# Performance work log

Measured on AMD Instinct MI355X. Metric: run time of the kernel, lower is better.

## Reference

```python
import jax, jax.numpy as jnp
import numpy as np

B, L, KD, ED, H = 8, 4096, 512, 1024, 8  # batch, seq, key_dim, embed_dim, n_heads
LN_EPS = 1e-5


def setup_inputs() -> dict:
    key = jax.random.key(0)
    ks = jax.random.split(key, 6)
    keys = jax.random.normal(ks[0], (B, L, KD), dtype=jnp.float32)
    values = jax.random.normal(ks[1], (B, L, ED), dtype=jnp.float32)
    # learned params
    query = jax.random.normal(ks[2], (H, 1, KD // H), dtype=jnp.float32) * 0.02
    k_bias = jax.random.normal(ks[3], (KD,), dtype=jnp.float32) / np.sqrt(KD).astype(np.float32)
    v_bias = jnp.zeros((ED,), dtype=jnp.float32)
    softmax_weight = 1.0 + 0.01 * jax.random.normal(ks[4], (H, 1, L + 1), dtype=jnp.float32)
    softmax_bias = 0.01 * jax.random.normal(ks[5], (H, 1, L + 1), dtype=jnp.float32)
    gamma = jnp.ones((ED,), dtype=jnp.float32)
    beta = jnp.zeros((ED,), dtype=jnp.float32)
    return {"keys": keys, "values": values, "query": query, "k_bias": k_bias,
            "v_bias": v_bias, "softmax_weight": softmax_weight,
            "softmax_bias": softmax_bias, "gamma": gamma, "beta": beta}


def reference(keys, values, query, k_bias, v_bias, softmax_weight, softmax_bias, gamma, beta):
    b = keys.shape[0]
    # append learned bias token to keys and values  -> [B, L+1, *]
    keys = jnp.concatenate([keys, jnp.broadcast_to(k_bias, (b, 1, k_bias.shape[0]))], axis=1)
    values = jnp.concatenate([values, jnp.broadcast_to(v_bias, (b, 1, v_bias.shape[0]))], axis=1)
    lp = keys.shape[1]
    # torch multihead_reshape is a raw contiguous view [B,L,C] -> [B*H, L, C/H]
    K = keys.reshape(b * H, lp, keys.shape[2] // H)      # [B*H, L+1, KD/H]
    V = values.reshape(b * H, lp, values.shape[2] // H)  # [B*H, L+1, ED/H]
    Q = jnp.tile(query, (b, 1, 1))                       # [B*H, 1, KD/H]
    scores = jnp.einsum('bqd,bld->bql', Q, K)            # [B*H, 1, L+1]
    scores = scores * jnp.tile(softmax_weight, (b, 1, 1)) + jnp.tile(softmax_bias, (b, 1, 1))
    attn = jax.nn.softmax(scores, axis=-1)               # [B*H, 1, L+1]
    A = jnp.einsum('bql,bld->bqd', attn, V)              # [B*H, 1, ED/H]
    A = A.reshape(b, 1, -1)                              # multihead_unshape -> [B, 1, ED]
    # LayerNorm over embed dim (torch default eps=1e-5, biased var)
    mean = jnp.mean(A, axis=-1, keepdims=True)
    var = jnp.var(A, axis=-1, keepdims=True)
    return (A - mean) * jax.lax.rsqrt(var + LN_EPS) * gamma + beta
```

## Files before the change

### kernel.cpp

```cpp
#include <hip/hip_runtime.h>

#define BATCH 8
#define LSEQ  4096
#define LP    4097
#define KDIM  512
#define EDIM  1024
#define NH    8
#define DK    64
#define DV    128
#define NG    64
#define NCH   16
#define KLIM  (LSEQ * KDIM)
#define VLIM  (LSEQ * EDIM)
#define LN_EPS 1e-5f

typedef float floatx4 __attribute__((ext_vector_type(4)));

#define STAGE_LOAD(S, rr) do {                                              \
    const int rk0 = (rr) + gid;                                             \
    const int rk1 = (rr) + 4 + gid;                                         \
    const int f0 = fheadk + rk0 * DK;                                       \
    const int f1 = fheadk + rk1 * DK;                                       \
    const float* p0 = (f0 < KLIM) ? (kp + f0) : (k_bias + (f0 - KLIM));     \
    const float* p1 = (f1 < KLIM) ? (kp + f1) : (k_bias + (f1 - KLIM));     \
    kv0##S = *reinterpret_cast<const floatx4*>(p0 + l16 * 4);               \
    kv1##S = *reinterpret_cast<const floatx4*>(p1 + l16 * 4);               \
    wv0##S = wptr[rk0]; bv0##S = bptr[rk0];                                 \
    wv1##S = wptr[rk1]; bv1##S = bptr[rk1];                                 \
    _Pragma("unroll")                                                       \
    for (int j = 0; j < 4; ++j) {                                           \
        const int fv = fheadv + ((rr) + 2 * j + hi) * DV;                   \
        const float* pv = (fv < VLIM) ? (vp + fv) : (v_bias + (fv - VLIM)); \
        vv##S[j] = *reinterpret_cast<const floatx4*>(pv + d0);              \
    }                                                                       \
} while (0)

#define STAGE_COMPUTE(S) do {                                               \
    float s0 = q.x * kv0##S.x + q.y * kv0##S.y + q.z * kv0##S.z + q.w * kv0##S.w; \
    float s1 = q.x * kv1##S.x + q.y * kv1##S.y + q.z * kv1##S.z + q.w * kv1##S.w; \
    s0 += __shfl_xor(s0, 1); s1 += __shfl_xor(s1, 1);                       \
    s0 += __shfl_xor(s0, 2); s1 += __shfl_xor(s1, 2);                       \
    s0 += __shfl_xor(s0, 4); s1 += __shfl_xor(s1, 4);                       \
    s0 += __shfl_xor(s0, 8); s1 += __shfl_xor(s1, 8);                       \
    const float e0 = __expf(s0 * wv0##S + bv0##S);                          \
    const float e1 = __expf(s1 * wv1##S + bv1##S);                          \
    z += e0 + e1;                                                           \
    const float w0 = __shfl(e0, 16 * hi, 64);                               \
    const float w1 = __shfl(e0, 16 * (2 + hi), 64);                         \
    const float w2 = __shfl(e1, 16 * hi, 64);                               \
    const float w3 = __shfl(e1, 16 * (2 + hi), 64);                         \
    a0 += w0 * vv##S[0].x; a1 += w0 * vv##S[0].y;                           \
    a2 += w0 * vv##S[0].z; a3 += w0 * vv##S[0].w;                           \
    a0 += w1 * vv##S[1].x; a1 += w1 * vv##S[1].y;                           \
    a2 += w1 * vv##S[1].z; a3 += w1 * vv##S[1].w;                           \
    a0 += w2 * vv##S[2].x; a1 += w2 * vv##S[2].y;                           \
    a2 += w2 * vv##S[2].z; a3 += w2 * vv##S[2].w;                           \
    a0 += w3 * vv##S[3].x; a1 += w3 * vv##S[3].y;                           \
    a2 += w3 * vv##S[3].z; a3 += w3 * vv##S[3].w;                           \
} while (0)

#define SB __builtin_amdgcn_sched_barrier(0)

__global__ __launch_bounds__(256, 4) void lqa_fused_kernel(
    const float* __restrict__ keys, const float* __restrict__ k_bias,
    const float* __restrict__ values, const float* __restrict__ v_bias,
    const float* __restrict__ query, const float* __restrict__ sw,
    const float* __restrict__ sb, float* __restrict__ partials,
    float* __restrict__ zstats)
{
    const int cg = blockIdx.x;
    const int g  = blockIdx.y;
    const int b = g >> 3, h = g & 7;
    const int t = threadIdx.x;
    const int w = t >> 6;
    const int lane = t & 63;
    const int R0 = cg * 256 + w * 64;

    __shared__ float red[4 * DV];
    __shared__ float zred[4];

    const int gid = lane >> 4, l16 = lane & 15;
    const int hi = (lane >> 5) & 1;
    const int d0 = (lane & 31) * 4;

    const float* kp = keys + (long long)b * (LSEQ * KDIM);
    const float* vp = values + (long long)b * (LSEQ * EDIM);
    const int fheadk = h * (LP * DK);
    const int fheadv = h * (LP * DV);
    const float* wptr = sw + h * LP;
    const float* bptr = sb + h * LP;
    const floatx4 q = *reinterpret_cast<const floatx4*>(query + h * DK + l16 * 4);

    floatx4 kv0A, kv1A, vvA[4];
    floatx4 kv0B, kv1B, vvB[4];
    float wv0A, wv1A, bv0A, bv1A;
    float wv0B, wv1B, bv0B, bv1B;
    float a0 = 0.f, a1 = 0.f, a2 = 0.f, a3 = 0.f, z = 0.f;

    STAGE_LOAD(A, R0 + 0);
    STAGE_LOAD(B, R0 + 8);
    SB;
    STAGE_COMPUTE(A);
    STAGE_LOAD(A, R0 + 16); SB; STAGE_COMPUTE(B);
    STAGE_LOAD(B, R0 + 24); SB; STAGE_COMPUTE(A);
    STAGE_LOAD(A, R0 + 32); SB; STAGE_COMPUTE(B);
    STAGE_LOAD(B, R0 + 40); SB; STAGE_COMPUTE(A);
    STAGE_LOAD(A, R0 + 48); SB; STAGE_COMPUTE(B);
    STAGE_LOAD(B, R0 + 56); SB; STAGE_COMPUTE(A);
    SB;
    STAGE_COMPUTE(B);

    a0 += __shfl_xor(a0, 32);
    a1 += __shfl_xor(a1, 32);
    a2 += __shfl_xor(a2, 32);
    a3 += __shfl_xor(a3, 32);
    z += __shfl_xor(z, 16);
    z += __shfl_xor(z, 32);

    if (lane < 32) {
        float* dst = red + w * DV + d0;
        dst[0] = a0; dst[1] = a1; dst[2] = a2; dst[3] = a3;
    }
    if (lane == 0) zred[w] = z;
    __syncthreads();
    if (t < DV) {
        const float sum = red[t] + red[DV + t] + red[2 * DV + t] + red[3 * DV + t];
        partials[((long long)(g * NCH + cg)) * DV + t] = sum;
    } else if (t == DV) {
        zstats[g * NCH + cg] = zred[0] + zred[1] + zred[2] + zred[3];
    }
}

__global__ __launch_bounds__(1024) void lqa_combine_ln_kernel(
    const float* __restrict__ partials, const float* __restrict__ zstats,
    const float* __restrict__ keys, const float* __restrict__ values,
    const float* __restrict__ k_bias, const float* __restrict__ v_bias,
    const float* __restrict__ query, const float* __restrict__ sw,
    const float* __restrict__ sb, const float* __restrict__ gamma,
    const float* __restrict__ beta, float* __restrict__ out)
{
    const int b = blockIdx.x;
    const int t = threadIdx.x;
    __shared__ float zh[NH];
    __shared__ float eb[NH];
    __shared__ float r1[16], r2[16];

    if (t < 128) {
        float zv = zstats[(b * NH + (t >> 4)) * NCH + (t & 15)];
        zv += __shfl_xor(zv, 1);
        zv += __shfl_xor(zv, 2);
        zv += __shfl_xor(zv, 4);
        zv += __shfl_xor(zv, 8);
        if ((t & 15) == 0) zh[t >> 4] = zv;
    } else if (t < 256) {
        const int tt = t - 128;
        const int h = tt >> 4, l16 = tt & 15;
        const floatx4 q = *reinterpret_cast<const floatx4*>(query + h * DK + l16 * 4);
        const int fk = h * (LP * DK) + LSEQ * DK;
        const float* kr = (fk < KLIM)
            ? keys + (long long)b * (LSEQ * KDIM) + fk
            : k_bias + (fk - KLIM);
        const floatx4 k = *reinterpret_cast<const floatx4*>(kr + l16 * 4);
        float s = q.x * k.x + q.y * k.y + q.z * k.z + q.w * k.w;
        s += __shfl_xor(s, 1);
        s += __shfl_xor(s, 2);
        s += __shfl_xor(s, 4);
        s += __shfl_xor(s, 8);
        if (l16 == 0) eb[h] = __expf(s * sw[h * LP + LSEQ] + sb[h * LP + LSEQ]);
    }
    __syncthreads();
    if (t < NH) zh[t] += eb[t];
    __syncthreads();

    const int h = t >> 7, d = t & 127;
    const float* src = partials + ((long long)((b * NH + h) * NCH)) * DV + d;
    float sum = 0.f;
#pragma unroll
    for (int c = 0; c < NCH; ++c) sum += src[c * DV];
    const int fv = h * (LP * DV) + LSEQ * DV + d;
    const float v4 = (fv < VLIM)
        ? values[(long long)b * (LSEQ * EDIM) + fv]
        : v_bias[fv - VLIM];
    const float av = (sum + eb[h] * v4) / zh[h];

    float s1 = av, s2 = av * av;
    s1 += __shfl_xor(s1, 1);  s2 += __shfl_xor(s2, 1);
    s1 += __shfl_xor(s1, 2);  s2 += __shfl_xor(s2, 2);
    s1 += __shfl_xor(s1, 4);  s2 += __shfl_xor(s2, 4);
    s1 += __shfl_xor(s1, 8);  s2 += __shfl_xor(s2, 8);
    s1 += __shfl_xor(s1, 16); s2 += __shfl_xor(s2, 16);
    s1 += __shfl_xor(s1, 32); s2 += __shfl_xor(s2, 32);
    if ((t & 63) == 0) { r1[t >> 6] = s1; r2[t >> 6] = s2; }
    __syncthreads();
    float fs1 = 0.f, fs2 = 0.f;
#pragma unroll
    for (int i = 0; i < 16; ++i) { fs1 += r1[i]; fs2 += r2[i]; }
    const float mean = fs1 * (1.0f / EDIM);
    const float var = fs2 * (1.0f / EDIM) - mean * mean;
    const float inv = rsqrtf(var + LN_EPS);
    out[(long long)b * EDIM + t] = (av - mean) * inv * gamma[t] + beta[t];
}

extern "C" void kernel_launch(void* const* d_in, const int* in_sizes, int n_in,
                              void* d_out, int out_size, void* d_ws, size_t ws_size,
                              hipStream_t stream) {
    const float* keys   = (const float*)d_in[0];
    const float* values = (const float*)d_in[1];
    const float* query  = (const float*)d_in[2];
    const float* k_bias = (const float*)d_in[3];
    const float* v_bias = (const float*)d_in[4];
    const float* sw     = (const float*)d_in[5];
    const float* sb     = (const float*)d_in[6];
    const float* gamma  = (const float*)d_in[7];
    const float* beta   = (const float*)d_in[8];
    float* out = (float*)d_out;

    float* ws = (float*)d_ws;
    float* partials = ws;
    float* zstats = ws + (long long)NG * NCH * DV;

    lqa_fused_kernel<<<dim3(NCH, NG), 256, 0, stream>>>(
        keys, k_bias, values, v_bias, query, sw, sb, partials, zstats);
    lqa_combine_ln_kernel<<<BATCH, 1024, 0, stream>>>(
        partials, zstats, keys, values, k_bias, v_bias, query, sw, sb,
        gamma, beta, out);
}
```

Baseline: 275.9 us.

## Split fused attention kernel into separate scores and AV kernels

The single fused kernel that computed scores, exponentials and the weighted value sum is split in two. The first kernel writes exp(score) for every row to a workspace buffer. The second loads those weights into shared memory and accumulates the weighted values, and also produces the softmax denominator partials. This removes the cross-lane shuffles and mixed key/value loads from the AV loop and gives each kernel a simpler access pattern. In exchange it adds a kernel launch and an extra round-trip of the score vector through global memory.

```diff
diff --git a/kernel.cpp b/kernel.cpp
--- a/kernel.cpp
+++ b/kernel.cpp
@@ -16,56 +16,79 @@
 
 typedef float floatx4 __attribute__((ext_vector_type(4)));
 
-#define STAGE_LOAD(S, rr) do {                                              \
-    const int rk0 = (rr) + gid;                                             \
-    const int rk1 = (rr) + 4 + gid;                                         \
-    const int f0 = fheadk + rk0 * DK;                                       \
-    const int f1 = fheadk + rk1 * DK;                                       \
-    const float* p0 = (f0 < KLIM) ? (kp + f0) : (k_bias + (f0 - KLIM));     \
-    const float* p1 = (f1 < KLIM) ? (kp + f1) : (k_bias + (f1 - KLIM));     \
-    kv0##S = *reinterpret_cast<const floatx4*>(p0 + l16 * 4);               \
-    kv1##S = *reinterpret_cast<const floatx4*>(p1 + l16 * 4);               \
-    wv0##S = wptr[rk0]; bv0##S = bptr[rk0];                                 \
-    wv1##S = wptr[rk1]; bv1##S = bptr[rk1];                                 \
+#define SB __builtin_amdgcn_sched_barrier(0)
+
+#define ALOAD(S, rr) do {                                                   \
+    const int row = (rr) + gid;                                             \
+    const int f = fheadk + row * DK;                                        \
+    const float* p = (f < KLIM) ? (kp + f) : (k_bias + (f - KLIM));         \
+    kv##S = *reinterpret_cast<const floatx4*>(p + l16 * 4);                 \
+    wv##S = wptr[row]; bv##S = bptr[row];                                   \
+} while (0)
+
+#define ACOMP(S, rr) do {                                                   \
+    float s = q.x * kv##S.x + q.y * kv##S.y + q.z * kv##S.z + q.w * kv##S.w;\
+    s += __shfl_xor(s, 1);                                                  \
+    s += __shfl_xor(s, 2);                                                  \
+    s += __shfl_xor(s, 4);                                                  \
+    s += __shfl_xor(s, 8);                                                  \
+    if (l16 == 0) eout[(rr) + gid] = __expf(s * wv##S + bv##S);             \
+} while (0)
+
+__global__ __launch_bounds__(256, 4) void lqa_scores_kernel(
+    const float* __restrict__ keys, const float* __restrict__ k_bias,
+    const float* __restrict__ query, const float* __restrict__ sw,
+    const float* __restrict__ sb, float* __restrict__ e)
+{
+    const int g = blockIdx.y;
+    const int b = g >> 3, h = g & 7;
+    const int t = threadIdx.x;
+    const int gid = t >> 4, l16 = t & 15;
+    const int row0 = blockIdx.x * 128;
+
+    const float* kp = keys + (long long)b * (LSEQ * KDIM);
+    const int fheadk = h * (LP * DK);
+    const float* wptr = sw + h * LP;
+    const float* bptr = sb + h * LP;
+    float* eout = e + (long long)g * LSEQ;
+    const floatx4 q = *reinterpret_cast<const floatx4*>(query + h * DK + l16 * 4);
+
+    floatx4 kvA, kvB;
+    float wvA, bvA, wvB, bvB;
+
+    ALOAD(A, row0 + 0); ALOAD(B, row0 + 16); SB;
+    ACOMP(A, row0 + 0);   ALOAD(A, row0 + 32);  SB;
+    ACOMP(B, row0 + 16);  ALOAD(B, row0 + 48);  SB;
+    ACOMP(A, row0 + 32);  ALOAD(A, row0 + 64);  SB;
+    ACOMP(B, row0 + 48);  ALOAD(B, row0 + 80);  SB;
+    ACOMP(A, row0 + 64);  ALOAD(A, row0 + 96);  SB;
+    ACOMP(B, row0 + 80);  ALOAD(B, row0 + 112); SB;
+    ACOMP(A, row0 + 96);  SB;
+    ACOMP(B, row0 + 112);
+}
+
+#define BLOAD(S, i0) do {                                                   \
     _Pragma("unroll")                                                       \
     for (int j = 0; j < 4; ++j) {                                           \
-        const int fv = fheadv + ((rr) + 2 * j + hi) * DV;                   \
-        const float* pv = (fv < VLIM) ? (vp + fv) : (v_bias + (fv - VLIM)); \
-        vv##S[j] = *reinterpret_cast<const floatx4*>(pv + d0);              \
+        const int row = row0 + srow + 8 * ((i0) + j);                       \
+        const int f = fheadv + row * DV;                                    \
+        const float* p = (f < VLIM) ? (vp + f) : (v_bias + (f - VLIM));     \
+        vv##S[j] = *reinterpret_cast<const floatx4*>(p + d0);               \
+        ev##S[j] = es[srow + 8 * ((i0) + j)];                               \
     }                                                                       \
 } while (0)
 
-#define STAGE_COMPUTE(S) do {                                               \
-    float s0 = q.x * kv0##S.x + q.y * kv0##S.y + q.z * kv0##S.z + q.w * kv0##S.w; \
-    float s1 = q.x * kv1##S.x + q.y * kv1##S.y + q.z * kv1##S.z + q.w * kv1##S.w; \
-    s0 += __shfl_xor(s0, 1); s1 += __shfl_xor(s1, 1);                       \
-    s0 += __shfl_xor(s0, 2); s1 += __shfl_xor(s1, 2);                       \
-    s0 += __shfl_xor(s0, 4); s1 += __shfl_xor(s1, 4);                       \
-    s0 += __shfl_xor(s0, 8); s1 += __shfl_xor(s1, 8);                       \
-    const float e0 = __expf(s0 * wv0##S + bv0##S);                          \
-    const float e1 = __expf(s1 * wv1##S + bv1##S);                          \
-    z += e0 + e1;                                                           \
-    const float w0 = __shfl(e0, 16 * hi, 64);                               \
-    const float w1 = __shfl(e0, 16 * (2 + hi), 64);                         \
-    const float w2 = __shfl(e1, 16 * hi, 64);                               \
-    const float w3 = __shfl(e1, 16 * (2 + hi), 64);                         \
-    a0 += w0 * vv##S[0].x; a1 += w0 * vv##S[0].y;                           \
-    a2 += w0 * vv##S[0].z; a3 += w0 * vv##S[0].w;                           \
-    a0 += w1 * vv##S[1].x; a1 += w1 * vv##S[1].y;                           \
-    a2 += w1 * vv##S[1].z; a3 += w1 * vv##S[1].w;                           \
-    a0 += w2 * vv##S[2].x; a1 += w2 * vv##S[2].y;                           \
-    a2 += w2 * vv##S[2].z; a3 += w2 * vv##S[2].w;                           \
-    a0 += w3 * vv##S[3].x; a1 += w3 * vv##S[3].y;                           \
-    a2 += w3 * vv##S[3].z; a3 += w3 * vv##S[3].w;                           \
-} while (0)
-
-#define SB __builtin_amdgcn_sched_barrier(0)
-
-__global__ __launch_bounds__(256, 4) void lqa_fused_kernel(
-    const float* __restrict__ keys, const float* __restrict__ k_bias,
+#define BCOMP(S) do {                                                       \
+    _Pragma("unroll")                                                       \
+    for (int j = 0; j < 4; ++j) {                                           \
+        a0 += ev##S[j] * vv##S[j].x; a1 += ev##S[j] * vv##S[j].y;           \
+        a2 += ev##S[j] * vv##S[j].z; a3 += ev##S[j] * vv##S[j].w;           \
+    }                                                                       \
+} while (0)
+
+__global__ __launch_bounds__(256, 4) void lqa_av_kernel(
     const float* __restrict__ values, const float* __restrict__ v_bias,
-    const float* __restrict__ query, const float* __restrict__ sw,
-    const float* __restrict__ sb, float* __restrict__ partials,
+    const float* __restrict__ e, float* __restrict__ partials,
     float* __restrict__ zstats)
 {
     const int cg = blockIdx.x;
@@ -74,60 +97,58 @@
     const int t = threadIdx.x;
     const int w = t >> 6;
     const int lane = t & 63;
-    const int R0 = cg * 256 + w * 64;
-
+    const int srow = t >> 5;
+    const int d0 = (t & 31) * 4;
+    const int row0 = cg * 256;
+
+    __shared__ float es[256];
     __shared__ float red[4 * DV];
-    __shared__ float zred[4];
-
-    const int gid = lane >> 4, l16 = lane & 15;
-    const int hi = (lane >> 5) & 1;
-    const int d0 = (lane & 31) * 4;
-
-    const float* kp = keys + (long long)b * (LSEQ * KDIM);
+
     const float* vp = values + (long long)b * (LSEQ * EDIM);
-    const int fheadk = h * (LP * DK);
     const int fheadv = h * (LP * DV);
-    const float* wptr = sw + h * LP;
-    const float* bptr = sb + h * LP;
-    const floatx4 q = *reinterpret_cast<const floatx4*>(query + h * DK + l16 * 4);
-
-    floatx4 kv0A, kv1A, vvA[4];
-    floatx4 kv0B, kv1B, vvB[4];
-    float wv0A, wv1A, bv0A, bv1A;
-    float wv0B, wv1B, bv0B, bv1B;
-    float a0 = 0.f, a1 = 0.f, a2 = 0.f, a3 = 0.f, z = 0.f;
-
-    STAGE_LOAD(A, R0 + 0);
-    STAGE_LOAD(B, R0 + 8);
-    SB;
-    STAGE_COMPUTE(A);
-    STAGE_LOAD(A, R0 + 16); SB; STAGE_COMPUTE(B);
-    STAGE_LOAD(B, R0 + 24); SB; STAGE_COMPUTE(A);
-    STAGE_LOAD(A, R0 + 32); SB; STAGE_COMPUTE(B);
-    STAGE_LOAD(B, R0 + 40); SB; STAGE_COMPUTE(A);
-    STAGE_LOAD(A, R0 + 48); SB; STAGE_COMPUTE(B);
-    STAGE_LOAD(B, R0 + 56); SB; STAGE_COMPUTE(A);
-    SB;
-    STAGE_COMPUTE(B);
+
+    es[t] = e[(long long)g * LSEQ + row0 + t];
+    __syncthreads();
+
+    floatx4 vvA[4], vvB[4];
+    float evA[4], evB[4];
+    float a0 = 0.f, a1 = 0.f, a2 = 0.f, a3 = 0.f;
+
+    BLOAD(A, 0); BLOAD(B, 4); SB;
+    BCOMP(A); BLOAD(A, 8);  SB;
+    BCOMP(B); BLOAD(B, 12); SB;
+    BCOMP(A); BLOAD(A, 16); SB;
+    BCOMP(B); BLOAD(B, 20); SB;
+    BCOMP(A); BLOAD(A, 24); SB;
+    BCOMP(B); BLOAD(B, 28); SB;
+    BCOMP(A); SB;
+    BCOMP(B);
 
     a0 += __shfl_xor(a0, 32);
     a1 += __shfl_xor(a1, 32);
     a2 += __shfl_xor(a2, 32);
     a3 += __shfl_xor(a3, 32);
-    z += __shfl_xor(z, 16);
-    z += __shfl_xor(z, 32);
+
+    float zp = 0.f;
+    if (t < 64) zp = es[t] + es[t + 64] + es[t + 128] + es[t + 192];
 
     if (lane < 32) {
         float* dst = red + w * DV + d0;
         dst[0] = a0; dst[1] = a1; dst[2] = a2; dst[3] = a3;
     }
-    if (lane == 0) zred[w] = z;
     __syncthreads();
     if (t < DV) {
         const float sum = red[t] + red[DV + t] + red[2 * DV + t] + red[3 * DV + t];
         partials[((long long)(g * NCH + cg)) * DV + t] = sum;
-    } else if (t == DV) {
-        zstats[g * NCH + cg] = zred[0] + zred[1] + zred[2] + zred[3];
+    }
+    if (t < 64) {
+        zp += __shfl_xor(zp, 1);
+        zp += __shfl_xor(zp, 2);
+        zp += __shfl_xor(zp, 4);
+        zp += __shfl_xor(zp, 8);
+        zp += __shfl_xor(zp, 16);
+        zp += __shfl_xor(zp, 32);
+        if (t == 0) zstats[g * NCH + cg] = zp;
     }
 }
 
@@ -218,9 +239,12 @@
     float* ws = (float*)d_ws;
     float* partials = ws;
     float* zstats = ws + (long long)NG * NCH * DV;
-
-    lqa_fused_kernel<<<dim3(NCH, NG), 256, 0, stream>>>(
-        keys, k_bias, values, v_bias, query, sw, sb, partials, zstats);
+    float* e = zstats + NG * NCH;
+
+    lqa_scores_kernel<<<dim3(32, NG), 256, 0, stream>>>(
+        keys, k_bias, query, sw, sb, e);
+    lqa_av_kernel<<<dim3(NCH, NG), 256, 0, stream>>>(
+        values, v_bias, e, partials, zstats);
     lqa_combine_ln_kernel<<<BATCH, 1024, 0, stream>>>(
         partials, zstats, keys, values, k_bias, v_bias, query, sw, sb,
         gamma, beta, out);
```

Result: faster. 252.4 us (-8.5%).
